# Kernel tuning notes

Hardware: AMD Instinct MI355X
Metric: run time of the kernel (lower is better)

## Reference

```python
import jax, jax.numpy as jnp
import numpy as np


def setup_inputs() -> dict:
    key = jax.random.key(0)
    ks = jax.random.split(key, 8)
    B, C, H, W = 4, 256, 64, 64
    Ci = C // 8  # inter_channels = 32
    x = jax.random.normal(ks[0], (B, C, H, W), dtype=jnp.float32)
    # 1x1 conv weights stored as [out, in] matrices (kernel size 1)
    sq = 1.0 / np.sqrt(C)
    Wq = jax.random.uniform(ks[1], (Ci, C), jnp.float32, -sq, sq)
    bq = jax.random.uniform(ks[2], (Ci,), jnp.float32, -sq, sq)
    Wk = jax.random.uniform(ks[3], (Ci, C), jnp.float32, -sq, sq)
    bk = jax.random.uniform(ks[4], (Ci,), jnp.float32, -sq, sq)
    Wv = jax.random.uniform(ks[5], (C, C), jnp.float32, -sq, sq)
    bv = jax.random.uniform(ks[6], (C,), jnp.float32, -sq, sq)
    # torch initializes gamma to zeros; use a nonzero value so output depends on attention path
    gamma = jnp.array([0.5], dtype=jnp.float32)
    return {"x": x, "Wq": Wq, "bq": bq, "Wk": Wk, "bk": bk, "Wv": Wv, "bv": bv, "gamma": gamma}


def reference(x, Wq, bq, Wk, bk, Wv, bv, gamma):
    B, C, H, W = x.shape
    N = H * W
    xf = x.reshape(B, C, N)                        # [B, C, N]
    # 1x1 convs == channel-mixing matmuls
    q = jnp.einsum('oc,bcn->bon', Wq, xf) + bq[None, :, None]   # [B, Ci, N]
    k = jnp.einsum('oc,bcn->bon', Wk, xf) + bk[None, :, None]   # [B, Ci, N]
    v = jnp.einsum('oc,bcn->bon', Wv, xf) + bv[None, :, None]   # [B, C,  N]
    # energy[b, n, m] = sum_c q[b, c, n] * k[b, c, m]  (no scaling, per DANet)
    energy = jnp.einsum('bcn,bcm->bnm', q, k)      # [B, N, N]
    attention = jax.nn.softmax(energy, axis=-1)    # softmax over keys m
    # out[b, c, n] = sum_m v[b, c, m] * attention[b, n, m]
    out = jnp.einsum('bcm,bnm->bcn', v, attention)
    out = out.reshape(B, C, H, W)
    return gamma[0] * out + x
```

## Files before the change

### kernel.cpp

```cpp
#include <hip/hip_runtime.h>
#include <hip/hip_bf16.h>
#include <math.h>

typedef __bf16 bf16x8 __attribute__((ext_vector_type(8)));
typedef float  floatx4 __attribute__((ext_vector_type(4)));

#define MFMA(a, b, c) __builtin_amdgcn_mfma_f32_16x16x32_bf16((a), (b), (c), 0, 0, 0)

__device__ __forceinline__ unsigned short f2bf(float f) {
  union { float f; unsigned u; } v; v.f = f;
  unsigned r = v.u + 0x7FFFu + ((v.u >> 16) & 1u);
  return (unsigned short)(r >> 16);
}
__device__ __forceinline__ float bf2f(unsigned short u) {
  union { unsigned u; float f; } v; v.u = ((unsigned)u) << 16;
  return v.f;
}

__global__ __launch_bounds__(256) void k_wconv(const float* __restrict__ Wq,
                                               const float* __restrict__ Wk,
                                               const float* __restrict__ Wv,
                                               unsigned short* __restrict__ Wall) {
  int i = blockIdx.x * 256 + threadIdx.x;
  int o = i >> 8, c = i & 255;
  float v = (o < 32) ? Wq[o * 256 + c]
          : (o < 64) ? Wk[(o - 32) * 256 + c]
                     : Wv[(o - 64) * 256 + c];
  Wall[i] = f2bf(v);
}

__global__ __launch_bounds__(256) void k_xpose(const float* __restrict__ x,
                                               unsigned short* __restrict__ xT) {
  int bid = blockIdx.x;
  int b = bid >> 8, rem = bid & 255;
  int nb = rem >> 2, cb = rem & 3;
  int n0 = nb * 64, c0 = cb * 64;
  int tid = threadIdx.x;
  __shared__ alignas(16) unsigned short T[64][72];
#pragma unroll
  for (int i = 0; i < 4; ++i) {
    int idx = tid + 256 * i;
    int r = idx >> 4, g = idx & 15;
    float4 d = *(const float4*)(x + ((size_t)b * 256 + c0 + r) * 4096 + n0 + g * 4);
    T[g * 4 + 0][r] = f2bf(d.x);
    T[g * 4 + 1][r] = f2bf(d.y);
    T[g * 4 + 2][r] = f2bf(d.z);
    T[g * 4 + 3][r] = f2bf(d.w);
  }
  __syncthreads();
#pragma unroll
  for (int i = 0; i < 2; ++i) {
    int idx = tid + 256 * i;
    int j = idx >> 3, g = idx & 7;
    *(uint4*)(xT + ((size_t)b * 4096 + n0 + j) * 256 + c0 + g * 8) =
        *(const uint4*)&T[j][g * 8];
  }
}

__global__ __launch_bounds__(64, 4) void k_proj(const unsigned short* __restrict__ xT,
                                                const unsigned short* __restrict__ Wall,
                                                const float* __restrict__ bq,
                                                const float* __restrict__ bk,
                                                const float* __restrict__ bv,
                                                unsigned short* __restrict__ qkT,
                                                unsigned short* __restrict__ vbf) {
  int b = blockIdx.x >> 9;
  int m0 = ((blockIdx.x >> 1) & 255) * 16;
  int h = blockIdx.x & 1;
  int lane = threadIdx.x & 63;
  int l15 = lane & 15, quad = lane >> 4;

  floatx4 acc[10];
#pragma unroll
  for (int tt = 0; tt < 10; ++tt) acc[tt] = floatx4{0.f, 0.f, 0.f, 0.f};

  const unsigned short* arow = xT + ((size_t)b * 4096 + m0 + l15) * 256;
#pragma unroll
  for (int ks = 0; ks < 8; ++ks) {
    bf16x8 a = *(const bf16x8*)(arow + ks * 32 + quad * 8);
#pragma unroll
    for (int tt = 0; tt < 10; ++tt) {
      int gt = (tt < 2) ? (h * 2 + tt) : (4 + h * 8 + (tt - 2));
      bf16x8 w = *(const bf16x8*)(Wall + (size_t)(gt * 16 + l15) * 256 + ks * 32 + quad * 8);
      acc[tt] = MFMA(a, w, acc[tt]);
    }
  }
#pragma unroll
  for (int tt = 0; tt < 2; ++tt) {
    int o = (h * 2 + tt) * 16 + l15;
    float bias = (o < 32) ? bq[o] : bk[o - 32];
#pragma unroll
    for (int r = 0; r < 4; ++r) {
      int m = m0 + quad * 4 + r;
      qkT[((size_t)b * 4096 + m) * 64 + o] = f2bf(acc[tt][r] + bias);
    }
  }
  __shared__ alignas(16) unsigned short Os[128][24];
#pragma unroll
  for (int tt = 2; tt < 10; ++tt) {
    int lr = (tt - 2) * 16 + l15;
    int c = h * 128 + lr;
    float bias = bv[c];
#pragma unroll
    for (int r = 0; r < 4; ++r)
      Os[lr][quad * 4 + r] = f2bf(acc[tt][r] + bias);
  }
  __syncthreads();
#pragma unroll
  for (int i = 0; i < 4; ++i) {
    int idx = threadIdx.x + 64 * i;
    int r = idx >> 1, g = idx & 1;
    int c = h * 128 + r;
    *(uint4*)(vbf + ((size_t)b * 256 + c) * 4096 + m0 + g * 8) = *(const uint4*)&Os[r][g * 8];
  }
}

__global__ __launch_bounds__(256, 3) void k_attn(const unsigned short* __restrict__ qkT,
                                                 const unsigned short* __restrict__ vbf,
                                                 unsigned short* __restrict__ Obf,
                                                 float* __restrict__ lsum) {
  const int b = blockIdx.x >> 8;
  const int s = (blockIdx.x >> 6) & 3;
  const int q0 = (blockIdx.x & 63) * 64;
  const int tid = threadIdx.x;
  const int wave = tid >> 6, lane = tid & 63;
  const int l15 = lane & 15, quad = lane >> 4;

  __shared__ alignas(16) unsigned short Kl[2][64][40];
  __shared__ alignas(16) unsigned short Pl[4][16][72];

  bf16x8 aq = *(const bf16x8*)(qkT + ((size_t)b * 4096 + q0 + wave * 16 + l15) * 64 + quad * 8);

  floatx4 O[4][4];
#pragma unroll
  for (int qt = 0; qt < 4; ++qt)
#pragma unroll
    for (int nt = 0; nt < 4; ++nt) O[qt][nt] = floatx4{0.f, 0.f, 0.f, 0.f};

  float l_part = 0.f;
  const floatx4 zero4 = {0.f, 0.f, 0.f, 0.f};

  const unsigned short* vrow = vbf + ((size_t)b * 256 + wave * 64) * 4096;

  {
    int r = tid >> 2, g = tid & 3;
    uint4 d = *(const uint4*)(qkT + ((size_t)b * 4096 + s * 1024 + r) * 64 + 32 + g * 8);
    *(uint4*)&Kl[0][r][g * 8] = d;
  }
  __syncthreads();

  for (int it = 0; it < 16; ++it) {
    const int m0 = (s * 16 + it) * 64;
    const int buf = it & 1;

    bf16x8 vb[4][2];
#pragma unroll
    for (int nt = 0; nt < 4; ++nt)
#pragma unroll
      for (int kk = 0; kk < 2; ++kk)
        vb[nt][kk] = *(const bf16x8*)(vrow + (size_t)(nt * 16 + l15) * 4096 + m0 + kk * 32 + quad * 8);

    floatx4 st[4];
#pragma unroll
    for (int t = 0; t < 4; ++t) {
      bf16x8 kb = *(const bf16x8*)&Kl[buf][t * 16 + l15][quad * 8];
      st[t] = MFMA(kb, aq, zero4);
    }
#pragma unroll
    for (int t = 0; t < 4; ++t) {
      float p0 = __expf(st[t][0]);
      float p1 = __expf(st[t][1]);
      float p2 = __expf(st[t][2]);
      float p3 = __expf(st[t][3]);
      l_part += (p0 + p1) + (p2 + p3);
      ushort4 pk = make_ushort4(f2bf(p0), f2bf(p1), f2bf(p2), f2bf(p3));
      *(ushort4*)&Pl[wave][l15][t * 16 + quad * 4] = pk;
    }

    if (it < 15) {
      int r = tid >> 2, g = tid & 3;
      uint4 d = *(const uint4*)(qkT + ((size_t)b * 4096 + m0 + 64 + r) * 64 + 32 + g * 8);
      *(uint4*)&Kl[buf ^ 1][r][g * 8] = d;
    }
    __syncthreads();

#pragma unroll
    for (int qt = 0; qt < 4; ++qt) {
      bf16x8 pa0 = *(const bf16x8*)&Pl[qt][l15][quad * 8];
      bf16x8 pa1 = *(const bf16x8*)&Pl[qt][l15][32 + quad * 8];
#pragma unroll
      for (int nt = 0; nt < 4; ++nt) {
        O[qt][nt] = MFMA(pa0, vb[nt][0], O[qt][nt]);
        O[qt][nt] = MFMA(pa1, vb[nt][1], O[qt][nt]);
      }
    }
    __syncthreads();
  }

  float lt = l_part;
  lt += __shfl_xor(lt, 16);
  lt += __shfl_xor(lt, 32);
  if (quad == 0)
    lsum[((size_t)s * 4 + b) * 4096 + q0 + wave * 16 + l15] = lt;

#pragma unroll
  for (int nt = 0; nt < 4; ++nt) {
    size_t crow = (((size_t)s * 4 + b) * 256 + wave * 64 + nt * 16 + l15) * 4096;
#pragma unroll
    for (int qt = 0; qt < 4; ++qt) {
      ushort4 ok = make_ushort4(f2bf(O[qt][nt][0]), f2bf(O[qt][nt][1]),
                                f2bf(O[qt][nt][2]), f2bf(O[qt][nt][3]));
      *(ushort4*)(Obf + crow + q0 + qt * 16 + quad * 4) = ok;
    }
  }
}

__global__ __launch_bounds__(256) void k_merge(const unsigned short* __restrict__ Obf,
                                               const float* __restrict__ lsum,
                                               const float* __restrict__ x,
                                               const float* __restrict__ gma,
                                               float* __restrict__ out) {
  int t = blockIdx.x * 256 + threadIdx.x;
  int n4 = t & 1023;
  int c = (t >> 10) & 255;
  int b = t >> 18;
  int n = n4 << 2;
  size_t xa = (((size_t)b * 256 + c) << 12) + n;
  float4 xv = *(const float4*)(x + xa);
  float L0 = 0.f, L1 = 0.f, L2 = 0.f, L3 = 0.f;
  float o0 = 0.f, o1 = 0.f, o2 = 0.f, o3 = 0.f;
#pragma unroll
  for (int s = 0; s < 4; ++s) {
    float4 ls = *(const float4*)(lsum + (((size_t)s * 4 + b) << 12) + n);
    L0 += ls.x; L1 += ls.y; L2 += ls.z; L3 += ls.w;
    ushort4 ov = *(const ushort4*)(Obf + ((((size_t)s * 4 + b) * 256 + c) << 12) + n);
    o0 += bf2f(ov.x); o1 += bf2f(ov.y); o2 += bf2f(ov.z); o3 += bf2f(ov.w);
  }
  float g = gma[0];
  float4 r;
  r.x = xv.x + g * o0 / L0;
  r.y = xv.y + g * o1 / L1;
  r.z = xv.z + g * o2 / L2;
  r.w = xv.w + g * o3 / L3;
  *(float4*)(out + xa) = r;
}

extern "C" void kernel_launch(void* const* d_in, const int* in_sizes, int n_in,
                              void* d_out, int out_size, void* d_ws, size_t ws_size,
                              hipStream_t stream) {
  const float* x   = (const float*)d_in[0];
  const float* Wq  = (const float*)d_in[1];
  const float* bq  = (const float*)d_in[2];
  const float* Wk  = (const float*)d_in[3];
  const float* bk  = (const float*)d_in[4];
  const float* Wv  = (const float*)d_in[5];
  const float* bv  = (const float*)d_in[6];
  const float* gma = (const float*)d_in[7];
  float* out = (float*)d_out;

  unsigned short* qkT  = (unsigned short*)d_ws;
  unsigned short* vbf  = qkT + (size_t)4 * 4096 * 64;
  unsigned short* Wall = vbf + (size_t)4 * 256 * 4096;
  unsigned short* xT   = Wall + (size_t)320 * 256;
  unsigned short* Obf  = xT;
  float* lsum = (float*)(Obf + (size_t)4 * 4 * 256 * 4096);

  k_wconv<<<320, 256, 0, stream>>>(Wq, Wk, Wv, Wall);
  k_xpose<<<1024, 256, 0, stream>>>(x, xT);
  k_proj<<<2048, 64, 0, stream>>>(xT, Wall, bq, bk, bv, qkT, vbf);
  k_attn<<<1024, 256, 0, stream>>>(qkT, vbf, Obf, lsum);
  k_merge<<<4096, 256, 0, stream>>>(Obf, lsum, x, gma, out);
}
```

Measured before the change: 191.9 us.

## Split attention over channel halves, double-buffer P, drop K LDS staging

```diff
diff --git a/kernel.cpp b/kernel.cpp
--- a/kernel.cpp
+++ b/kernel.cpp
@@ -15,6 +15,11 @@
 __device__ __forceinline__ float bf2f(unsigned short u) {
   union { unsigned u; float f; } v; v.u = ((unsigned)u) << 16;
   return v.f;
+}
+__device__ __forceinline__ unsigned pk2bf(float a, float b) {
+  __hip_bfloat162 h = __float22bfloat162_rn(make_float2(a, b));
+  union { __hip_bfloat162 h; unsigned u; } v; v.h = h;
+  return v.u;
 }
 
 __global__ __launch_bounds__(256) void k_wconv(const float* __restrict__ Wq,
@@ -64,72 +69,72 @@
                                                 const float* __restrict__ bv,
                                                 unsigned short* __restrict__ qkT,
                                                 unsigned short* __restrict__ vbf) {
-  int b = blockIdx.x >> 9;
-  int m0 = ((blockIdx.x >> 1) & 255) * 16;
-  int h = blockIdx.x & 1;
+  int b = blockIdx.x >> 10;
+  int m0 = ((blockIdx.x >> 2) & 255) * 16;
+  int h = blockIdx.x & 3;
   int lane = threadIdx.x & 63;
   int l15 = lane & 15, quad = lane >> 4;
 
-  floatx4 acc[10];
-#pragma unroll
-  for (int tt = 0; tt < 10; ++tt) acc[tt] = floatx4{0.f, 0.f, 0.f, 0.f};
+  floatx4 acc[5];
+#pragma unroll
+  for (int tt = 0; tt < 5; ++tt) acc[tt] = floatx4{0.f, 0.f, 0.f, 0.f};
 
   const unsigned short* arow = xT + ((size_t)b * 4096 + m0 + l15) * 256;
 #pragma unroll
   for (int ks = 0; ks < 8; ++ks) {
     bf16x8 a = *(const bf16x8*)(arow + ks * 32 + quad * 8);
 #pragma unroll
-    for (int tt = 0; tt < 10; ++tt) {
-      int gt = (tt < 2) ? (h * 2 + tt) : (4 + h * 8 + (tt - 2));
+    for (int tt = 0; tt < 5; ++tt) {
+      int gt = (tt == 0) ? h : (4 + h * 4 + (tt - 1));
       bf16x8 w = *(const bf16x8*)(Wall + (size_t)(gt * 16 + l15) * 256 + ks * 32 + quad * 8);
       acc[tt] = MFMA(a, w, acc[tt]);
     }
   }
-#pragma unroll
-  for (int tt = 0; tt < 2; ++tt) {
-    int o = (h * 2 + tt) * 16 + l15;
+  {
+    int o = h * 16 + l15;
     float bias = (o < 32) ? bq[o] : bk[o - 32];
 #pragma unroll
     for (int r = 0; r < 4; ++r) {
       int m = m0 + quad * 4 + r;
-      qkT[((size_t)b * 4096 + m) * 64 + o] = f2bf(acc[tt][r] + bias);
-    }
-  }
-  __shared__ alignas(16) unsigned short Os[128][24];
-#pragma unroll
-  for (int tt = 2; tt < 10; ++tt) {
-    int lr = (tt - 2) * 16 + l15;
-    int c = h * 128 + lr;
-    float bias = bv[c];
+      qkT[((size_t)b * 4096 + m) * 64 + o] = f2bf(acc[0][r] + bias);
+    }
+  }
+  __shared__ alignas(16) unsigned short Os[64][24];
+#pragma unroll
+  for (int tt = 1; tt < 5; ++tt) {
+    int lr = (tt - 1) * 16 + l15;
+    float bias = bv[h * 64 + lr];
 #pragma unroll
     for (int r = 0; r < 4; ++r)
       Os[lr][quad * 4 + r] = f2bf(acc[tt][r] + bias);
   }
   __syncthreads();
 #pragma unroll
-  for (int i = 0; i < 4; ++i) {
-    int idx = threadIdx.x + 64 * i;
+  for (int i = 0; i < 2; ++i) {
+    int idx = lane + 64 * i;
     int r = idx >> 1, g = idx & 1;
-    int c = h * 128 + r;
-    *(uint4*)(vbf + ((size_t)b * 256 + c) * 4096 + m0 + g * 8) = *(const uint4*)&Os[r][g * 8];
-  }
-}
-
-__global__ __launch_bounds__(256, 3) void k_attn(const unsigned short* __restrict__ qkT,
+    *(uint4*)(vbf + ((size_t)b * 256 + h * 64 + r) * 4096 + m0 + g * 8) =
+        *(const uint4*)&Os[r][g * 8];
+  }
+}
+
+__global__ __launch_bounds__(128, 4) void k_attn(const unsigned short* __restrict__ qkT,
                                                  const unsigned short* __restrict__ vbf,
                                                  unsigned short* __restrict__ Obf,
                                                  float* __restrict__ lsum) {
-  const int b = blockIdx.x >> 8;
-  const int s = (blockIdx.x >> 6) & 3;
+  const int b = blockIdx.x >> 9;
+  const int s = (blockIdx.x >> 7) & 3;
+  const int chalf = (blockIdx.x >> 6) & 1;
   const int q0 = (blockIdx.x & 63) * 64;
   const int tid = threadIdx.x;
-  const int wave = tid >> 6, lane = tid & 63;
+  const int w = tid >> 6, lane = tid & 63;
   const int l15 = lane & 15, quad = lane >> 4;
 
-  __shared__ alignas(16) unsigned short Kl[2][64][40];
-  __shared__ alignas(16) unsigned short Pl[4][16][72];
-
-  bf16x8 aq = *(const bf16x8*)(qkT + ((size_t)b * 4096 + q0 + wave * 16 + l15) * 64 + quad * 8);
+  __shared__ alignas(16) unsigned short Pl[2][4][8][16][8];
+
+  const unsigned short* qbase = qkT + (size_t)b * 4096 * 64;
+  bf16x8 aq0 = *(const bf16x8*)(qbase + (size_t)(q0 + (2 * w + 0) * 16 + l15) * 64 + quad * 8);
+  bf16x8 aq1 = *(const bf16x8*)(qbase + (size_t)(q0 + (2 * w + 1) * 16 + l15) * 64 + quad * 8);
 
   floatx4 O[4][4];
 #pragma unroll
@@ -137,22 +142,20 @@
 #pragma unroll
     for (int nt = 0; nt < 4; ++nt) O[qt][nt] = floatx4{0.f, 0.f, 0.f, 0.f};
 
-  float l_part = 0.f;
+  float l0 = 0.f, l1 = 0.f;
   const floatx4 zero4 = {0.f, 0.f, 0.f, 0.f};
 
-  const unsigned short* vrow = vbf + ((size_t)b * 256 + wave * 64) * 4096;
-
-  {
-    int r = tid >> 2, g = tid & 3;
-    uint4 d = *(const uint4*)(qkT + ((size_t)b * 4096 + s * 1024 + r) * 64 + 32 + g * 8);
-    *(uint4*)&Kl[0][r][g * 8] = d;
-  }
-  __syncthreads();
+  const unsigned short* vrow = vbf + ((size_t)b * 256 + chalf * 128 + w * 64) * 4096;
+  const unsigned short* krow = qbase + 32;
 
   for (int it = 0; it < 16; ++it) {
     const int m0 = (s * 16 + it) * 64;
-    const int buf = it & 1;
-
+    const int pb = it & 1;
+
+    bf16x8 kb[4];
+#pragma unroll
+    for (int t = 0; t < 4; ++t)
+      kb[t] = *(const bf16x8*)(krow + (size_t)(m0 + t * 16 + l15) * 64 + quad * 8);
     bf16x8 vb[4][2];
 #pragma unroll
     for (int nt = 0; nt < 4; ++nt)
@@ -160,57 +163,52 @@
       for (int kk = 0; kk < 2; ++kk)
         vb[nt][kk] = *(const bf16x8*)(vrow + (size_t)(nt * 16 + l15) * 4096 + m0 + kk * 32 + quad * 8);
 
-    floatx4 st[4];
-#pragma unroll
-    for (int t = 0; t < 4; ++t) {
-      bf16x8 kb = *(const bf16x8*)&Kl[buf][t * 16 + l15][quad * 8];
-      st[t] = MFMA(kb, aq, zero4);
-    }
-#pragma unroll
-    for (int t = 0; t < 4; ++t) {
-      float p0 = __expf(st[t][0]);
-      float p1 = __expf(st[t][1]);
-      float p2 = __expf(st[t][2]);
-      float p3 = __expf(st[t][3]);
-      l_part += (p0 + p1) + (p2 + p3);
-      ushort4 pk = make_ushort4(f2bf(p0), f2bf(p1), f2bf(p2), f2bf(p3));
-      *(ushort4*)&Pl[wave][l15][t * 16 + quad * 4] = pk;
-    }
-
-    if (it < 15) {
-      int r = tid >> 2, g = tid & 3;
-      uint4 d = *(const uint4*)(qkT + ((size_t)b * 4096 + m0 + 64 + r) * 64 + 32 + g * 8);
-      *(uint4*)&Kl[buf ^ 1][r][g * 8] = d;
+    const int qk_hi = quad >> 1, qk_lo = (quad & 1) * 4;
+#pragma unroll
+    for (int g = 0; g < 2; ++g) {
+#pragma unroll
+      for (int t = 0; t < 4; ++t) {
+        floatx4 st = MFMA(kb[t], g ? aq1 : aq0, zero4);
+        float p0 = __expf(st[0]);
+        float p1 = __expf(st[1]);
+        float p2 = __expf(st[2]);
+        float p3 = __expf(st[3]);
+        float sm = (p0 + p1) + (p2 + p3);
+        if (g) l1 += sm; else l0 += sm;
+        uint2 pk = make_uint2(pk2bf(p0, p1), pk2bf(p2, p3));
+        *(uint2*)&Pl[pb][2 * w + g][2 * t + qk_hi][l15][qk_lo] = pk;
+      }
     }
     __syncthreads();
 
 #pragma unroll
     for (int qt = 0; qt < 4; ++qt) {
-      bf16x8 pa0 = *(const bf16x8*)&Pl[qt][l15][quad * 8];
-      bf16x8 pa1 = *(const bf16x8*)&Pl[qt][l15][32 + quad * 8];
+      bf16x8 pa0 = *(const bf16x8*)&Pl[pb][qt][quad][l15][0];
+      bf16x8 pa1 = *(const bf16x8*)&Pl[pb][qt][quad + 4][l15][0];
 #pragma unroll
       for (int nt = 0; nt < 4; ++nt) {
         O[qt][nt] = MFMA(pa0, vb[nt][0], O[qt][nt]);
         O[qt][nt] = MFMA(pa1, vb[nt][1], O[qt][nt]);
       }
     }
-    __syncthreads();
-  }
-
-  float lt = l_part;
-  lt += __shfl_xor(lt, 16);
-  lt += __shfl_xor(lt, 32);
-  if (quad == 0)
-    lsum[((size_t)s * 4 + b) * 4096 + q0 + wave * 16 + l15] = lt;
+  }
+
+  l0 += __shfl_xor(l0, 16); l0 += __shfl_xor(l0, 32);
+  l1 += __shfl_xor(l1, 16); l1 += __shfl_xor(l1, 32);
+  if (chalf == 0 && quad == 0) {
+    size_t base = ((size_t)s * 4 + b) * 4096 + q0;
+    lsum[base + (2 * w + 0) * 16 + l15] = l0;
+    lsum[base + (2 * w + 1) * 16 + l15] = l1;
+  }
 
 #pragma unroll
   for (int nt = 0; nt < 4; ++nt) {
-    size_t crow = (((size_t)s * 4 + b) * 256 + wave * 64 + nt * 16 + l15) * 4096;
+    size_t crow = (((size_t)s * 4 + b) * 256 + chalf * 128 + w * 64 + nt * 16 + l15) * 4096;
 #pragma unroll
     for (int qt = 0; qt < 4; ++qt) {
-      ushort4 ok = make_ushort4(f2bf(O[qt][nt][0]), f2bf(O[qt][nt][1]),
-                                f2bf(O[qt][nt][2]), f2bf(O[qt][nt][3]));
-      *(ushort4*)(Obf + crow + q0 + qt * 16 + quad * 4) = ok;
+      uint2 ok = make_uint2(pk2bf(O[qt][nt][0], O[qt][nt][1]),
+                            pk2bf(O[qt][nt][2], O[qt][nt][3]));
+      *(uint2*)(Obf + crow + q0 + qt * 16 + quad * 4) = ok;
     }
   }
 }
@@ -267,7 +265,7 @@
 
   k_wconv<<<320, 256, 0, stream>>>(Wq, Wk, Wv, Wall);
   k_xpose<<<1024, 256, 0, stream>>>(x, xT);
-  k_proj<<<2048, 64, 0, stream>>>(xT, Wall, bq, bk, bv, qkT, vbf);
-  k_attn<<<1024, 256, 0, stream>>>(qkT, vbf, Obf, lsum);
+  k_proj<<<4096, 64, 0, stream>>>(xT, Wall, bq, bk, bv, qkT, vbf);
+  k_attn<<<2048, 128, 0, stream>>>(qkT, vbf, Obf, lsum);
   k_merge<<<4096, 256, 0, stream>>>(Obf, lsum, x, gma, out);
 }
```

Result: slower. 283.5 us (+47.7%).
